# Kernel optimization log

Measured on AMD Instinct MI355X. Metric: run time of the kernel, lower is better.

## Reference

```python
import jax, jax.numpy as jnp
import numpy as np

B = 65536
NREQ = 2097152
NVEH = 1048576
NPAS = 2097152
E = 4194304


def _xavier(key, fi, fo):
    gain = 5.0 / 3.0  # tanh gain
    std = gain * np.sqrt(2.0 / (fi + fo))
    return jax.random.normal(key, (fi, fo), dtype=jnp.float32) * std


def scatter_mean(x, idx, num_segments):
    s = jax.ops.segment_sum(x, idx, num_segments=num_segments)
    c = jax.ops.segment_sum(jnp.ones((x.shape[0], 1), x.dtype), idx, num_segments=num_segments)
    return s / jnp.maximum(c, 1.0)


def setup_inputs() -> dict:
    key = jax.random.key(0)
    ks = jax.random.split(key, 16)
    inp = {
        "requests_x": jax.random.normal(ks[0], (NREQ, 10), dtype=jnp.float32),
        "requests_x_batch": jnp.sort(jax.random.randint(ks[1], (NREQ,), 0, B)),
        "vehicles_x": jax.random.normal(ks[2], (NVEH, 8), dtype=jnp.float32),
        "vehicles_x_batch": jnp.sort(jax.random.randint(ks[3], (NVEH,), 0, B)),
        "passengers_x": jax.random.normal(ks[4], (NPAS, 10), dtype=jnp.float32),
        "veh2pas_receiver_edge_index": jax.random.randint(ks[5], (E,), 0, NPAS),
        "veh2pas_sender_edge_index": jax.random.randint(ks[6], (E,), 0, NVEH),
        "req2veh_receiver_start_index": jax.random.randint(ks[7], (B,), 0, NVEH),
        "W_req": _xavier(ks[8], 10, 16), "b_req": jnp.zeros((16,), jnp.float32),
        "W_veh": _xavier(ks[9], 8, 16), "b_veh": jnp.zeros((16,), jnp.float32),
        "W_pas": _xavier(ks[10], 10, 16), "b_pas": jnp.zeros((16,), jnp.float32),
        "W1": _xavier(ks[11], 64, 64), "b1": jnp.zeros((64,), jnp.float32),
        "W2": _xavier(ks[12], 64, 64), "b2": jnp.zeros((64,), jnp.float32),
        "W3": _xavier(ks[13], 64, 1), "b3": jnp.zeros((1,), jnp.float32),
    }
    return inp


def reference(requests_x, requests_x_batch, vehicles_x, vehicles_x_batch, passengers_x,
              veh2pas_receiver_edge_index, veh2pas_sender_edge_index,
              req2veh_receiver_start_index,
              W_req, b_req, W_veh, b_veh, W_pas, b_pas, W1, b1, W2, b2, W3, b3):
    # per-node-type small MLPs
    req_feat = jnp.tanh(requests_x @ W_req + b_req)            # [NREQ,16]
    req_mean = scatter_mean(req_feat, requests_x_batch, B)      # [B,16]
    veh_feat = jnp.tanh(vehicles_x @ W_veh + b_veh)             # [NVEH,16]
    pas_feat = jnp.tanh(passengers_x @ W_pas + b_pas)           # [NPAS,16]
    # gather passengers along edges, mean-pool onto vehicles
    pas_mean = scatter_mean(pas_feat[veh2pas_receiver_edge_index],
                            veh2pas_sender_edge_index, NVEH)    # [NVEH,16]
    ego_feat = jnp.concatenate([veh_feat, pas_mean], axis=-1)[req2veh_receiver_start_index]  # [B,32]
    veh_mean = scatter_mean(veh_feat, vehicles_x_batch, B)      # [B,16]
    action_feat = jnp.concatenate([req_mean, ego_feat, veh_mean], axis=-1)  # [B,64]
    h = jnp.tanh(action_feat @ W1 + b1)
    h = jnp.tanh(h @ W2 + b2)
    return h @ W3 + b3                                          # [B,1]
```

## Files before the change

### kernel.cpp

```cpp
#include <hip/hip_runtime.h>
#include <cstddef>
#include <cstdint>

#define TPB 256
#define BATCH 65536
#define NREQ 2097152
#define NVEH 1048576
#define NPAS 2097152
#define NEDGE 4194304
#define CAP 32
#define RANK_NEG ((int)0x80808080)

__device__ __forceinline__ float fast_tanh(float x) {
    float e = __expf(2.0f * x);
    return 1.0f - 2.0f / (e + 1.0f);
}
__device__ __forceinline__ float4 tanh4(float4 v) {
    return make_float4(fast_tanh(v.x), fast_tanh(v.y), fast_tanh(v.z), fast_tanh(v.w));
}

__global__ __launch_bounds__(TPB) void k_bounds(
    const int* __restrict__ req_batch, const int* __restrict__ veh_batch,
    const int* __restrict__ req2veh,
    int* __restrict__ seg_req, int* __restrict__ seg_veh,
    unsigned char* __restrict__ mark, int* __restrict__ rank, int* __restrict__ cnt)
{
    int i = blockIdx.x * TPB + threadIdx.x;
    {
        int cur = req_batch[i];
        int prev = (i == 0) ? -1 : req_batch[i - 1];
        for (int b = prev + 1; b <= cur; ++b) seg_req[b] = i;
        if (i == NREQ - 1)
            for (int b = cur + 1; b <= BATCH; ++b) seg_req[b] = NREQ;
    }
    if (i < NVEH) {
        int cur = veh_batch[i];
        int prev = (i == 0) ? -1 : veh_batch[i - 1];
        for (int b = prev + 1; b <= cur; ++b) seg_veh[b] = i;
        if (i == NVEH - 1)
            for (int b = cur + 1; b <= BATCH; ++b) seg_veh[b] = NVEH;
    }
    if (i < BATCH) {
        int v = req2veh[i];
        mark[v] = 1;
        int old = atomicCAS(&rank[v], RANK_NEG, RANK_NEG + 1);
        if (old == RANK_NEG) rank[v] = atomicAdd(cnt, 1);
    }
}

template<int F>
__device__ __forceinline__ void seg_mean_reg(
    const float* __restrict__ x, const int* __restrict__ seg,
    const float* __restrict__ W, const float* __restrict__ bias,
    float* __restrict__ mean_out, int b, int q)
{
    float4 wq[F];
    #pragma unroll
    for (int i = 0; i < F; ++i)
        wq[i] = *reinterpret_cast<const float4*>(&W[i*16 + q*4]);
    float4 bq = reinterpret_cast<const float4*>(bias)[q];

    int lo = seg[b];
    int hi = seg[b + 1];
    float4 s = make_float4(0.f, 0.f, 0.f, 0.f);
    for (int r = lo; r < hi; ++r) {
        float xr[F];
        if constexpr (F == 10) {
            const float2* p2 = reinterpret_cast<const float2*>(x + (size_t)r * 10);
            #pragma unroll
            for (int i = 0; i < 5; ++i) { float2 t = p2[i]; xr[2*i] = t.x; xr[2*i+1] = t.y; }
        } else {
            const float4* p4 = reinterpret_cast<const float4*>(x + (size_t)r * 8);
            float4 t0 = p4[0], t1 = p4[1];
            xr[0]=t0.x; xr[1]=t0.y; xr[2]=t0.z; xr[3]=t0.w;
            xr[4]=t1.x; xr[5]=t1.y; xr[6]=t1.z; xr[7]=t1.w;
        }
        float4 acc = bq;
        #pragma unroll
        for (int i = 0; i < F; ++i) {
            acc.x = fmaf(xr[i], wq[i].x, acc.x);
            acc.y = fmaf(xr[i], wq[i].y, acc.y);
            acc.z = fmaf(xr[i], wq[i].z, acc.z);
            acc.w = fmaf(xr[i], wq[i].w, acc.w);
        }
        float4 t = tanh4(acc);
        s.x += t.x; s.y += t.y; s.z += t.z; s.w += t.w;
    }
    float inv = 1.0f / fmaxf((float)(hi - lo), 1.0f);
    float4 o = make_float4(s.x*inv, s.y*inv, s.z*inv, s.w*inv);
    reinterpret_cast<float4*>(mean_out)[(size_t)b*4 + q] = o;
}

__global__ __launch_bounds__(TPB, 4) void k_phase1(
    const float* __restrict__ requests_x, const int* __restrict__ seg_req,
    const float* __restrict__ vehicles_x, const int* __restrict__ seg_veh,
    const float* __restrict__ W_req, const float* __restrict__ b_req,
    const float* __restrict__ W_veh, const float* __restrict__ b_veh,
    float* __restrict__ req_mean, float* __restrict__ veh_mean)
{
    const int NB_REQ = BATCH * 4 / TPB;
    int blk = blockIdx.x;
    if (blk < NB_REQ) {
        int t = blk * TPB + threadIdx.x;
        seg_mean_reg<10>(requests_x, seg_req, W_req, b_req, req_mean, t >> 2, t & 3);
    } else {
        int t = (blk - NB_REQ) * TPB + threadIdx.x;
        seg_mean_reg<8>(vehicles_x, seg_veh, W_veh, b_veh, veh_mean, t >> 2, t & 3);
    }
}

__global__ __launch_bounds__(TPB) void k_edge(
    const int* __restrict__ send, const int* __restrict__ recv,
    const unsigned char* __restrict__ mark, const int* __restrict__ rank,
    int* __restrict__ deg, int* __restrict__ bucket)
{
    int e = blockIdx.x * TPB + threadIdx.x;
    int v = send[e];
    if (mark[v]) {
        int r = rank[v];
        int slot = atomicAdd(&deg[r], 1);
        if (slot < CAP) bucket[(size_t)r * CAP + slot] = recv[e];
    }
}

__global__ __launch_bounds__(TPB, 3) void k_final(
    const float* __restrict__ req_mean, const float* __restrict__ veh_mean,
    const int* __restrict__ rank, const int* __restrict__ deg,
    const int* __restrict__ bucket, const float* __restrict__ pas_x,
    const float* __restrict__ vehicles_x, const int* __restrict__ req2veh,
    const float* __restrict__ W_veh, const float* __restrict__ b_veh,
    const float* __restrict__ W_pas, const float* __restrict__ b_pas,
    const float* __restrict__ W1, const float* __restrict__ b1,
    const float* __restrict__ W2, const float* __restrict__ b2,
    const float* __restrict__ W3, const float* __restrict__ b3,
    float* __restrict__ out)
{
    __shared__ __align__(16) float sW1[4096];
    __shared__ __align__(16) float sW2[4096];
    __shared__ float sW3[64];
    __shared__ float sb1[64];
    __shared__ float sb2[64];

    int tid = threadIdx.x;
    {
        const float4* s1 = reinterpret_cast<const float4*>(W1);
        const float4* s2 = reinterpret_cast<const float4*>(W2);
        float4* d1 = reinterpret_cast<float4*>(sW1);
        float4* d2 = reinterpret_cast<float4*>(sW2);
        for (int i = tid; i < 1024; i += TPB) { d1[i] = s1[i]; d2[i] = s2[i]; }
        if (tid < 64) { sW3[tid] = W3[tid]; sb1[tid] = b1[tid]; sb2[tid] = b2[tid]; }
    }
    __syncthreads();

    int q = tid & 3;
    int b = blockIdx.x * (TPB / 4) + (tid >> 2);
    int lane = tid & 63;
    int lbase = lane & ~3;

    float a[64];
    {
        const float4* rs = reinterpret_cast<const float4*>(req_mean) + (size_t)b*4;
        const float4* vs = reinterpret_cast<const float4*>(veh_mean) + (size_t)b*4;
        #pragma unroll
        for (int j4 = 0; j4 < 4; ++j4) {
            float4 t = rs[j4];
            a[4*j4+0]=t.x; a[4*j4+1]=t.y; a[4*j4+2]=t.z; a[4*j4+3]=t.w;
            float4 u = vs[j4];
            a[48+4*j4+0]=u.x; a[48+4*j4+1]=u.y; a[48+4*j4+2]=u.z; a[48+4*j4+3]=u.w;
        }
    }
    int v = req2veh[b];

    float4 fv;
    {
        float4 wv[8];
        #pragma unroll
        for (int i = 0; i < 8; ++i)
            wv[i] = *reinterpret_cast<const float4*>(&W_veh[i*16 + q*4]);
        float4 bv = reinterpret_cast<const float4*>(b_veh)[q];
        const float4* vp = reinterpret_cast<const float4*>(vehicles_x + (size_t)v*8);
        float4 t0 = vp[0], t1 = vp[1];
        float vx[8] = {t0.x,t0.y,t0.z,t0.w,t1.x,t1.y,t1.z,t1.w};
        float4 acc = bv;
        #pragma unroll
        for (int i = 0; i < 8; ++i) {
            acc.x = fmaf(vx[i], wv[i].x, acc.x); acc.y = fmaf(vx[i], wv[i].y, acc.y);
            acc.z = fmaf(vx[i], wv[i].z, acc.z); acc.w = fmaf(vx[i], wv[i].w, acc.w);
        }
        fv = tanh4(acc);
    }

    float4 fp;
    {
        float4 wp[10];
        #pragma unroll
        for (int i = 0; i < 10; ++i)
            wp[i] = *reinterpret_cast<const float4*>(&W_pas[i*16 + q*4]);
        float4 bp = reinterpret_cast<const float4*>(b_pas)[q];
        int r = rank[v];
        int d = deg[r];
        int n = min(d, CAP);
        const int* bk = bucket + (size_t)r * CAP;
        float4 ps = make_float4(0.f, 0.f, 0.f, 0.f);
        for (int s = 0; s < n; ++s) {
            int p = bk[s];
            float px[10];
            const float2* pp = reinterpret_cast<const float2*>(pas_x + (size_t)p * 10);
            #pragma unroll
            for (int i = 0; i < 5; ++i) { float2 t = pp[i]; px[2*i] = t.x; px[2*i+1] = t.y; }
            float4 acc = bp;
            #pragma unroll
            for (int i = 0; i < 10; ++i) {
                acc.x = fmaf(px[i], wp[i].x, acc.x); acc.y = fmaf(px[i], wp[i].y, acc.y);
                acc.z = fmaf(px[i], wp[i].z, acc.z); acc.w = fmaf(px[i], wp[i].w, acc.w);
            }
            float4 t = tanh4(acc);
            ps.x += t.x; ps.y += t.y; ps.z += t.z; ps.w += t.w;
        }
        float inv = 1.0f / fmaxf((float)d, 1.0f);
        fp = make_float4(ps.x*inv, ps.y*inv, ps.z*inv, ps.w*inv);
    }

    #pragma unroll
    for (int src = 0; src < 4; ++src) {
        a[16+4*src+0] = __shfl(fv.x, lbase+src);
        a[16+4*src+1] = __shfl(fv.y, lbase+src);
        a[16+4*src+2] = __shfl(fv.z, lbase+src);
        a[16+4*src+3] = __shfl(fv.w, lbase+src);
        a[32+4*src+0] = __shfl(fp.x, lbase+src);
        a[32+4*src+1] = __shfl(fp.y, lbase+src);
        a[32+4*src+2] = __shfl(fp.z, lbase+src);
        a[32+4*src+3] = __shfl(fp.w, lbase+src);
    }

    const float4* W1v = reinterpret_cast<const float4*>(sW1);
    const float4* W2v = reinterpret_cast<const float4*>(sW2);

    float hq[16];
    {
        float4 acc[4];
        #pragma unroll
        for (int jj = 0; jj < 4; ++jj)
            acc[jj] = *reinterpret_cast<const float4*>(&sb1[q*16 + jj*4]);
        #pragma unroll
        for (int k = 0; k < 64; ++k) {
            float ak = a[k];
            #pragma unroll
            for (int jj = 0; jj < 4; ++jj) {
                float4 w = W1v[k*16 + q*4 + jj];
                acc[jj].x = fmaf(ak, w.x, acc[jj].x); acc[jj].y = fmaf(ak, w.y, acc[jj].y);
                acc[jj].z = fmaf(ak, w.z, acc[jj].z); acc[jj].w = fmaf(ak, w.w, acc[jj].w);
            }
        }
        #pragma unroll
        for (int jj = 0; jj < 4; ++jj) {
            float4 t = tanh4(acc[jj]);
            hq[4*jj+0]=t.x; hq[4*jj+1]=t.y; hq[4*jj+2]=t.z; hq[4*jj+3]=t.w;
        }
    }
    #pragma unroll
    for (int src = 0; src < 4; ++src)
        #pragma unroll
        for (int jj = 0; jj < 16; ++jj)
            a[src*16 + jj] = __shfl(hq[jj], lbase + src);

    float o;
    {
        float4 acc[4];
        #pragma unroll
        for (int jj = 0; jj < 4; ++jj)
            acc[jj] = *reinterpret_cast<const float4*>(&sb2[q*16 + jj*4]);
        #pragma unroll
        for (int k = 0; k < 64; ++k) {
            float ak = a[k];
            #pragma unroll
            for (int jj = 0; jj < 4; ++jj) {
                float4 w = W2v[k*16 + q*4 + jj];
                acc[jj].x = fmaf(ak, w.x, acc[jj].x); acc[jj].y = fmaf(ak, w.y, acc[jj].y);
                acc[jj].z = fmaf(ak, w.z, acc[jj].z); acc[jj].w = fmaf(ak, w.w, acc[jj].w);
            }
        }
        o = 0.0f;
        #pragma unroll
        for (int jj = 0; jj < 4; ++jj) {
            float4 t = tanh4(acc[jj]);
            o = fmaf(t.x, sW3[q*16+4*jj+0], o);
            o = fmaf(t.y, sW3[q*16+4*jj+1], o);
            o = fmaf(t.z, sW3[q*16+4*jj+2], o);
            o = fmaf(t.w, sW3[q*16+4*jj+3], o);
        }
    }
    o += __shfl_xor(o, 1);
    o += __shfl_xor(o, 2);
    if (q == 0) out[b] = o + b3[0];
}

extern "C" void kernel_launch(void* const* d_in, const int* in_sizes, int n_in,
                              void* d_out, int out_size, void* d_ws, size_t ws_size,
                              hipStream_t stream) {
    const float* requests_x = (const float*)d_in[0];
    const int*   req_batch  = (const int*)d_in[1];
    const float* vehicles_x = (const float*)d_in[2];
    const int*   veh_batch  = (const int*)d_in[3];
    const float* pas_x      = (const float*)d_in[4];
    const int*   recv       = (const int*)d_in[5];
    const int*   send       = (const int*)d_in[6];
    const int*   req2veh    = (const int*)d_in[7];
    const float* W_req = (const float*)d_in[8];
    const float* b_req = (const float*)d_in[9];
    const float* W_veh = (const float*)d_in[10];
    const float* b_veh = (const float*)d_in[11];
    const float* W_pas = (const float*)d_in[12];
    const float* b_pas = (const float*)d_in[13];
    const float* W1 = (const float*)d_in[14];
    const float* b1 = (const float*)d_in[15];
    const float* W2 = (const float*)d_in[16];
    const float* b2 = (const float*)d_in[17];
    const float* W3 = (const float*)d_in[18];
    const float* b3 = (const float*)d_in[19];
    float* out = (float*)d_out;

    char* ws = (char*)d_ws;
    float*         req_mean = (float*)        (ws + 0);
    float*         veh_mean = (float*)        (ws + (4u<<20));
    int*           seg_req  = (int*)          (ws + (8u<<20));
    int*           seg_veh  = (int*)          (ws + (9u<<20));
    unsigned char* mark     = (unsigned char*)(ws + (10u<<20));
    int*           rank     = (int*)          (ws + (11u<<20));
    int*           deg      = (int*)          (ws + (15u<<20));
    int*           cnt      = (int*)          (ws + (15u<<20) + (256u<<10));
    int*           bucket   = (int*)          (ws + (16u<<20));

    hipMemsetAsync(mark, 0, NVEH, stream);
    hipMemsetAsync(rank, 0x80, NVEH * sizeof(int), stream);
    hipMemsetAsync(deg, 0, (256u<<10) + 64, stream);

    k_bounds<<<NREQ/TPB, TPB, 0, stream>>>(
        req_batch, veh_batch, req2veh, seg_req, seg_veh, mark, rank, cnt);

    k_phase1<<<(BATCH*4/TPB)*2, TPB, 0, stream>>>(
        requests_x, seg_req, vehicles_x, seg_veh,
        W_req, b_req, W_veh, b_veh, req_mean, veh_mean);

    k_edge<<<NEDGE/TPB, TPB, 0, stream>>>(send, recv, mark, rank, deg, bucket);

    k_final<<<BATCH*4/TPB, TPB, 0, stream>>>(
        req_mean, veh_mean, rank, deg, bucket, pas_x,
        vehicles_x, req2veh, W_veh, b_veh, W_pas, b_pas,
        W1, b1, W2, b2, W3, b3, out);
}
```

Measured before the change: 174.4 us.

## Stage segment rows in shared memory and use bitmask for vehicle marks

Phase 1 now has each block cover 64 contiguous segments. It loads their rows cooperatively and coalesced into LDS tiles of 512 rows, and each 4-thread team then reduces its own segment from shared memory. Before, each thread walked its segment's rows with strided global loads. Separately, the per-vehicle byte mark array becomes a packed bitmask set with atomicOr, which shrinks the memset and the random lookups in the edge kernel to 128KB. The costs are extra __syncthreads per tile, atomics when setting bits, and reduced occupancy from LDS use.

```diff
diff --git a/kernel.cpp b/kernel.cpp
--- a/kernel.cpp
+++ b/kernel.cpp
@@ -6,10 +6,11 @@
 #define BATCH 65536
 #define NREQ 2097152
 #define NVEH 1048576
-#define NPAS 2097152
 #define NEDGE 4194304
 #define CAP 32
 #define RANK_NEG ((int)0x80808080)
+#define RT 512
+#define SPB 64
 
 __device__ __forceinline__ float fast_tanh(float x) {
     float e = __expf(2.0f * x);
@@ -23,7 +24,7 @@
     const int* __restrict__ req_batch, const int* __restrict__ veh_batch,
     const int* __restrict__ req2veh,
     int* __restrict__ seg_req, int* __restrict__ seg_veh,
-    unsigned char* __restrict__ mark, int* __restrict__ rank, int* __restrict__ cnt)
+    unsigned* __restrict__ markbits, int* __restrict__ rank, int* __restrict__ cnt)
 {
     int i = blockIdx.x * TPB + threadIdx.x;
     {
@@ -42,81 +43,99 @@
     }
     if (i < BATCH) {
         int v = req2veh[i];
-        mark[v] = 1;
+        atomicOr(&markbits[v >> 5], 1u << (v & 31));
         int old = atomicCAS(&rank[v], RANK_NEG, RANK_NEG + 1);
         if (old == RANK_NEG) rank[v] = atomicAdd(cnt, 1);
     }
 }
 
 template<int F>
-__device__ __forceinline__ void seg_mean_reg(
+__device__ __forceinline__ void phase1_work(
     const float* __restrict__ x, const int* __restrict__ seg,
     const float* __restrict__ W, const float* __restrict__ bias,
-    float* __restrict__ mean_out, int b, int q)
-{
+    float* __restrict__ mout, int b0, float2* sX, int tid)
+{
+    constexpr int FP2 = F / 2;
+    int team = tid >> 2, q = tid & 3;
+    int b = b0 + team;
+    int lo = seg[b], hi = seg[b + 1];
+    int lo0 = seg[b0], hi_all = seg[b0 + SPB];
+
     float4 wq[F];
     #pragma unroll
     for (int i = 0; i < F; ++i)
-        wq[i] = *reinterpret_cast<const float4*>(&W[i*16 + q*4]);
+        wq[i] = *reinterpret_cast<const float4*>(&W[i * 16 + q * 4]);
     float4 bq = reinterpret_cast<const float4*>(bias)[q];
 
-    int lo = seg[b];
-    int hi = seg[b + 1];
     float4 s = make_float4(0.f, 0.f, 0.f, 0.f);
-    for (int r = lo; r < hi; ++r) {
-        float xr[F];
+
+    for (int rb = lo0; rb < hi_all; rb += RT) {
+        int nr = min(RT, hi_all - rb);
+        __syncthreads();
         if constexpr (F == 10) {
-            const float2* p2 = reinterpret_cast<const float2*>(x + (size_t)r * 10);
-            #pragma unroll
-            for (int i = 0; i < 5; ++i) { float2 t = p2[i]; xr[2*i] = t.x; xr[2*i+1] = t.y; }
+            const float2* src = reinterpret_cast<const float2*>(x + (size_t)rb * 10);
+            for (int i = tid; i < nr * 5; i += TPB) sX[i] = src[i];
         } else {
-            const float4* p4 = reinterpret_cast<const float4*>(x + (size_t)r * 8);
-            float4 t0 = p4[0], t1 = p4[1];
-            xr[0]=t0.x; xr[1]=t0.y; xr[2]=t0.z; xr[3]=t0.w;
-            xr[4]=t1.x; xr[5]=t1.y; xr[6]=t1.z; xr[7]=t1.w;
-        }
-        float4 acc = bq;
-        #pragma unroll
-        for (int i = 0; i < F; ++i) {
-            acc.x = fmaf(xr[i], wq[i].x, acc.x);
-            acc.y = fmaf(xr[i], wq[i].y, acc.y);
-            acc.z = fmaf(xr[i], wq[i].z, acc.z);
-            acc.w = fmaf(xr[i], wq[i].w, acc.w);
-        }
-        float4 t = tanh4(acc);
-        s.x += t.x; s.y += t.y; s.z += t.z; s.w += t.w;
+            const float2* src = reinterpret_cast<const float2*>(x + (size_t)rb * 8);
+            for (int idx = tid; idx < nr * 4; idx += TPB) {
+                int rr = idx >> 2, i = idx & 3;
+                sX[rr * 5 + i] = src[idx];
+            }
+        }
+        __syncthreads();
+
+        int r0 = max(lo, rb), r1 = min(hi, rb + nr);
+        for (int r = r0; r < r1; ++r) {
+            const float2* row = &sX[(r - rb) * 5];
+            float xr[F];
+            #pragma unroll
+            for (int i = 0; i < FP2; ++i) {
+                float2 t = row[i];
+                xr[2 * i] = t.x; xr[2 * i + 1] = t.y;
+            }
+            float4 acc = bq;
+            #pragma unroll
+            for (int i = 0; i < F; ++i) {
+                acc.x = fmaf(xr[i], wq[i].x, acc.x);
+                acc.y = fmaf(xr[i], wq[i].y, acc.y);
+                acc.z = fmaf(xr[i], wq[i].z, acc.z);
+                acc.w = fmaf(xr[i], wq[i].w, acc.w);
+            }
+            float4 t = tanh4(acc);
+            s.x += t.x; s.y += t.y; s.z += t.z; s.w += t.w;
+        }
     }
     float inv = 1.0f / fmaxf((float)(hi - lo), 1.0f);
-    float4 o = make_float4(s.x*inv, s.y*inv, s.z*inv, s.w*inv);
-    reinterpret_cast<float4*>(mean_out)[(size_t)b*4 + q] = o;
-}
-
-__global__ __launch_bounds__(TPB, 4) void k_phase1(
+    float4 o = make_float4(s.x * inv, s.y * inv, s.z * inv, s.w * inv);
+    reinterpret_cast<float4*>(mout)[(size_t)b * 4 + q] = o;
+}
+
+__global__ __launch_bounds__(TPB) void k_phase1(
     const float* __restrict__ requests_x, const int* __restrict__ seg_req,
     const float* __restrict__ vehicles_x, const int* __restrict__ seg_veh,
     const float* __restrict__ W_req, const float* __restrict__ b_req,
     const float* __restrict__ W_veh, const float* __restrict__ b_veh,
     float* __restrict__ req_mean, float* __restrict__ veh_mean)
 {
-    const int NB_REQ = BATCH * 4 / TPB;
+    __shared__ __align__(16) float2 sX[RT * 5];
+    const int NBR = BATCH / SPB;
     int blk = blockIdx.x;
-    if (blk < NB_REQ) {
-        int t = blk * TPB + threadIdx.x;
-        seg_mean_reg<10>(requests_x, seg_req, W_req, b_req, req_mean, t >> 2, t & 3);
-    } else {
-        int t = (blk - NB_REQ) * TPB + threadIdx.x;
-        seg_mean_reg<8>(vehicles_x, seg_veh, W_veh, b_veh, veh_mean, t >> 2, t & 3);
-    }
+    if (blk < NBR)
+        phase1_work<10>(requests_x, seg_req, W_req, b_req, req_mean,
+                        blk * SPB, sX, threadIdx.x);
+    else
+        phase1_work<8>(vehicles_x, seg_veh, W_veh, b_veh, veh_mean,
+                       (blk - NBR) * SPB, sX, threadIdx.x);
 }
 
 __global__ __launch_bounds__(TPB) void k_edge(
     const int* __restrict__ send, const int* __restrict__ recv,
-    const unsigned char* __restrict__ mark, const int* __restrict__ rank,
+    const unsigned* __restrict__ markbits, const int* __restrict__ rank,
     int* __restrict__ deg, int* __restrict__ bucket)
 {
     int e = blockIdx.x * TPB + threadIdx.x;
     int v = send[e];
-    if (mark[v]) {
+    if ((markbits[v >> 5] >> (v & 31)) & 1u) {
         int r = rank[v];
         int slot = atomicAdd(&deg[r], 1);
         if (slot < CAP) bucket[(size_t)r * CAP + slot] = recv[e];
@@ -321,28 +340,28 @@
     float* out = (float*)d_out;
 
     char* ws = (char*)d_ws;
-    float*         req_mean = (float*)        (ws + 0);
-    float*         veh_mean = (float*)        (ws + (4u<<20));
-    int*           seg_req  = (int*)          (ws + (8u<<20));
-    int*           seg_veh  = (int*)          (ws + (9u<<20));
-    unsigned char* mark     = (unsigned char*)(ws + (10u<<20));
-    int*           rank     = (int*)          (ws + (11u<<20));
-    int*           deg      = (int*)          (ws + (15u<<20));
-    int*           cnt      = (int*)          (ws + (15u<<20) + (256u<<10));
-    int*           bucket   = (int*)          (ws + (16u<<20));
-
-    hipMemsetAsync(mark, 0, NVEH, stream);
+    float*    req_mean = (float*)   (ws + 0);
+    float*    veh_mean = (float*)   (ws + (4u<<20));
+    int*      seg_req  = (int*)     (ws + (8u<<20));
+    int*      seg_veh  = (int*)     (ws + (9u<<20));
+    unsigned* markbits = (unsigned*)(ws + (10u<<20));
+    int*      rank     = (int*)     (ws + (11u<<20));
+    int*      deg      = (int*)     (ws + (15u<<20));
+    int*      cnt      = (int*)     (ws + (15u<<20) + (256u<<10));
+    int*      bucket   = (int*)     (ws + (16u<<20));
+
+    hipMemsetAsync(markbits, 0, NVEH / 8, stream);
     hipMemsetAsync(rank, 0x80, NVEH * sizeof(int), stream);
     hipMemsetAsync(deg, 0, (256u<<10) + 64, stream);
 
     k_bounds<<<NREQ/TPB, TPB, 0, stream>>>(
-        req_batch, veh_batch, req2veh, seg_req, seg_veh, mark, rank, cnt);
-
-    k_phase1<<<(BATCH*4/TPB)*2, TPB, 0, stream>>>(
+        req_batch, veh_batch, req2veh, seg_req, seg_veh, markbits, rank, cnt);
+
+    k_phase1<<<(BATCH/SPB)*2, TPB, 0, stream>>>(
         requests_x, seg_req, vehicles_x, seg_veh,
         W_req, b_req, W_veh, b_veh, req_mean, veh_mean);
 
-    k_edge<<<NEDGE/TPB, TPB, 0, stream>>>(send, recv, mark, rank, deg, bucket);
+    k_edge<<<NEDGE/TPB, TPB, 0, stream>>>(send, recv, markbits, rank, deg, bucket);
 
     k_final<<<BATCH*4/TPB, TPB, 0, stream>>>(
         req_mean, veh_mean, rank, deg, bucket, pas_x,
```

New measurement: 223.3 us. +28.0%, slower.

## Merge segment-mean and edge kernels, bitmask marks, vectorize loads and unroll gathers

Applied to the files above, without the earlier changes.

Folds the request/vehicle segment-mean kernel and the edge-bucketing kernel into one launch so the two independent phases can run concurrently. The byte mark array becomes a bitmask set with atomicOr, which shrinks the memset and the lookup footprint. The bounds and edge kernels now process four items per thread with int4 loads. The segment-mean and passenger-gather loops are unrolled by four to get more loads in flight. The cost is more register pressure, extra atomics on shared bitmask words, and a new workspace layout.

```diff
diff --git a/kernel.cpp b/kernel.cpp
--- a/kernel.cpp
+++ b/kernel.cpp
@@ -6,7 +6,6 @@
 #define BATCH 65536
 #define NREQ 2097152
 #define NVEH 1048576
-#define NPAS 2097152
 #define NEDGE 4194304
 #define CAP 32
 #define RANK_NEG ((int)0x80808080)
@@ -17,34 +16,64 @@
 }
 __device__ __forceinline__ float4 tanh4(float4 v) {
     return make_float4(fast_tanh(v.x), fast_tanh(v.y), fast_tanh(v.z), fast_tanh(v.w));
+}
+
+template<int F>
+__device__ __forceinline__ void load_row(const float* __restrict__ x, int r, float* xr) {
+    if constexpr (F == 10) {
+        const float2* p = reinterpret_cast<const float2*>(x + (size_t)r * 10);
+        #pragma unroll
+        for (int i = 0; i < 5; ++i) { float2 t = p[i]; xr[2*i] = t.x; xr[2*i+1] = t.y; }
+    } else {
+        const float4* p = reinterpret_cast<const float4*>(x + (size_t)r * 8);
+        float4 a = p[0], b = p[1];
+        xr[0]=a.x; xr[1]=a.y; xr[2]=a.z; xr[3]=a.w;
+        xr[4]=b.x; xr[5]=b.y; xr[6]=b.z; xr[7]=b.w;
+    }
 }
 
 __global__ __launch_bounds__(TPB) void k_bounds(
     const int* __restrict__ req_batch, const int* __restrict__ veh_batch,
     const int* __restrict__ req2veh,
     int* __restrict__ seg_req, int* __restrict__ seg_veh,
-    unsigned char* __restrict__ mark, int* __restrict__ rank, int* __restrict__ cnt)
+    unsigned* __restrict__ markbits, int* __restrict__ rank, int* __restrict__ cnt)
 {
-    int i = blockIdx.x * TPB + threadIdx.x;
-    {
-        int cur = req_batch[i];
-        int prev = (i == 0) ? -1 : req_batch[i - 1];
-        for (int b = prev + 1; b <= cur; ++b) seg_req[b] = i;
-        if (i == NREQ - 1)
-            for (int b = cur + 1; b <= BATCH; ++b) seg_req[b] = NREQ;
-    }
-    if (i < NVEH) {
-        int cur = veh_batch[i];
-        int prev = (i == 0) ? -1 : veh_batch[i - 1];
-        for (int b = prev + 1; b <= cur; ++b) seg_veh[b] = i;
-        if (i == NVEH - 1)
-            for (int b = cur + 1; b <= BATCH; ++b) seg_veh[b] = NVEH;
-    }
-    if (i < BATCH) {
-        int v = req2veh[i];
-        mark[v] = 1;
-        int old = atomicCAS(&rank[v], RANK_NEG, RANK_NEG + 1);
-        if (old == RANK_NEG) rank[v] = atomicAdd(cnt, 1);
+    int t = blockIdx.x * TPB + threadIdx.x;
+    int i0 = t * 4;
+    {
+        int4 c = *reinterpret_cast<const int4*>(req_batch + i0);
+        int prev = (i0 == 0) ? -1 : req_batch[i0 - 1];
+        int vals[4] = {c.x, c.y, c.z, c.w};
+        #pragma unroll
+        for (int u = 0; u < 4; ++u) {
+            for (int b = prev + 1; b <= vals[u]; ++b) seg_req[b] = i0 + u;
+            prev = vals[u];
+        }
+        if (i0 + 4 == NREQ)
+            for (int b = prev + 1; b <= BATCH; ++b) seg_req[b] = NREQ;
+    }
+    if (i0 < NVEH) {
+        int4 c = *reinterpret_cast<const int4*>(veh_batch + i0);
+        int prev = (i0 == 0) ? -1 : veh_batch[i0 - 1];
+        int vals[4] = {c.x, c.y, c.z, c.w};
+        #pragma unroll
+        for (int u = 0; u < 4; ++u) {
+            for (int b = prev + 1; b <= vals[u]; ++b) seg_veh[b] = i0 + u;
+            prev = vals[u];
+        }
+        if (i0 + 4 == NVEH)
+            for (int b = prev + 1; b <= BATCH; ++b) seg_veh[b] = NVEH;
+    }
+    if (i0 < BATCH) {
+        int4 vv = *reinterpret_cast<const int4*>(req2veh + i0);
+        int vs[4] = {vv.x, vv.y, vv.z, vv.w};
+        #pragma unroll
+        for (int u = 0; u < 4; ++u) {
+            int v = vs[u];
+            atomicOr(&markbits[v >> 5], 1u << (v & 31));
+            int old = atomicCAS(&rank[v], RANK_NEG, RANK_NEG + 1);
+            if (old == RANK_NEG) rank[v] = atomicAdd(cnt, 1);
+        }
     }
 }
 
@@ -63,18 +92,29 @@
     int lo = seg[b];
     int hi = seg[b + 1];
     float4 s = make_float4(0.f, 0.f, 0.f, 0.f);
-    for (int r = lo; r < hi; ++r) {
+
+    int r = lo;
+    for (; r + 4 <= hi; r += 4) {
+        float xr[4][F];
+        #pragma unroll
+        for (int u = 0; u < 4; ++u) load_row<F>(x, r + u, xr[u]);
+        #pragma unroll
+        for (int u = 0; u < 4; ++u) {
+            float4 acc = bq;
+            #pragma unroll
+            for (int i = 0; i < F; ++i) {
+                acc.x = fmaf(xr[u][i], wq[i].x, acc.x);
+                acc.y = fmaf(xr[u][i], wq[i].y, acc.y);
+                acc.z = fmaf(xr[u][i], wq[i].z, acc.z);
+                acc.w = fmaf(xr[u][i], wq[i].w, acc.w);
+            }
+            float4 tv = tanh4(acc);
+            s.x += tv.x; s.y += tv.y; s.z += tv.z; s.w += tv.w;
+        }
+    }
+    for (; r < hi; ++r) {
         float xr[F];
-        if constexpr (F == 10) {
-            const float2* p2 = reinterpret_cast<const float2*>(x + (size_t)r * 10);
-            #pragma unroll
-            for (int i = 0; i < 5; ++i) { float2 t = p2[i]; xr[2*i] = t.x; xr[2*i+1] = t.y; }
-        } else {
-            const float4* p4 = reinterpret_cast<const float4*>(x + (size_t)r * 8);
-            float4 t0 = p4[0], t1 = p4[1];
-            xr[0]=t0.x; xr[1]=t0.y; xr[2]=t0.z; xr[3]=t0.w;
-            xr[4]=t1.x; xr[5]=t1.y; xr[6]=t1.z; xr[7]=t1.w;
-        }
+        load_row<F>(x, r, xr);
         float4 acc = bq;
         #pragma unroll
         for (int i = 0; i < F; ++i) {
@@ -83,43 +123,50 @@
             acc.z = fmaf(xr[i], wq[i].z, acc.z);
             acc.w = fmaf(xr[i], wq[i].w, acc.w);
         }
-        float4 t = tanh4(acc);
-        s.x += t.x; s.y += t.y; s.z += t.z; s.w += t.w;
+        float4 tv = tanh4(acc);
+        s.x += tv.x; s.y += tv.y; s.z += tv.z; s.w += tv.w;
     }
     float inv = 1.0f / fmaxf((float)(hi - lo), 1.0f);
     float4 o = make_float4(s.x*inv, s.y*inv, s.z*inv, s.w*inv);
     reinterpret_cast<float4*>(mean_out)[(size_t)b*4 + q] = o;
 }
 
-__global__ __launch_bounds__(TPB, 4) void k_phase1(
+#define NB_REQ (BATCH/64)
+#define NB_VEH (BATCH/64)
+#define NB_P1  (NB_REQ + NB_VEH)
+#define NB_EDGE (NEDGE/(TPB*4))
+
+__global__ __launch_bounds__(TPB, 4) void k_mid(
     const float* __restrict__ requests_x, const int* __restrict__ seg_req,
     const float* __restrict__ vehicles_x, const int* __restrict__ seg_veh,
     const float* __restrict__ W_req, const float* __restrict__ b_req,
     const float* __restrict__ W_veh, const float* __restrict__ b_veh,
-    float* __restrict__ req_mean, float* __restrict__ veh_mean)
-{
-    const int NB_REQ = BATCH * 4 / TPB;
-    int blk = blockIdx.x;
-    if (blk < NB_REQ) {
-        int t = blk * TPB + threadIdx.x;
-        seg_mean_reg<10>(requests_x, seg_req, W_req, b_req, req_mean, t >> 2, t & 3);
-    } else {
-        int t = (blk - NB_REQ) * TPB + threadIdx.x;
-        seg_mean_reg<8>(vehicles_x, seg_veh, W_veh, b_veh, veh_mean, t >> 2, t & 3);
-    }
-}
-
-__global__ __launch_bounds__(TPB) void k_edge(
+    float* __restrict__ req_mean, float* __restrict__ veh_mean,
     const int* __restrict__ send, const int* __restrict__ recv,
-    const unsigned char* __restrict__ mark, const int* __restrict__ rank,
+    const unsigned* __restrict__ markbits, const int* __restrict__ rank,
     int* __restrict__ deg, int* __restrict__ bucket)
 {
-    int e = blockIdx.x * TPB + threadIdx.x;
-    int v = send[e];
-    if (mark[v]) {
-        int r = rank[v];
-        int slot = atomicAdd(&deg[r], 1);
-        if (slot < CAP) bucket[(size_t)r * CAP + slot] = recv[e];
+    int blk = blockIdx.x;
+    int tid = threadIdx.x;
+    if (blk < NB_REQ) {
+        int t = blk * TPB + tid;
+        seg_mean_reg<10>(requests_x, seg_req, W_req, b_req, req_mean, t >> 2, t & 3);
+    } else if (blk < NB_P1) {
+        int t = (blk - NB_REQ) * TPB + tid;
+        seg_mean_reg<8>(vehicles_x, seg_veh, W_veh, b_veh, veh_mean, t >> 2, t & 3);
+    } else {
+        int e4 = (blk - NB_P1) * TPB + tid;
+        int4 sv = reinterpret_cast<const int4*>(send)[e4];
+        int vv[4] = {sv.x, sv.y, sv.z, sv.w};
+        #pragma unroll
+        for (int u = 0; u < 4; ++u) {
+            int v = vv[u];
+            if ((markbits[v >> 5] >> (v & 31)) & 1u) {
+                int rk = rank[v];
+                int slot = atomicAdd(&deg[rk], 1);
+                if (slot < CAP) bucket[(size_t)rk * CAP + slot] = recv[e4 * 4 + u];
+            }
+        }
     }
 }
 
@@ -178,9 +225,8 @@
         for (int i = 0; i < 8; ++i)
             wv[i] = *reinterpret_cast<const float4*>(&W_veh[i*16 + q*4]);
         float4 bv = reinterpret_cast<const float4*>(b_veh)[q];
-        const float4* vp = reinterpret_cast<const float4*>(vehicles_x + (size_t)v*8);
-        float4 t0 = vp[0], t1 = vp[1];
-        float vx[8] = {t0.x,t0.y,t0.z,t0.w,t1.x,t1.y,t1.z,t1.w};
+        float vx[8];
+        load_row<8>(vehicles_x, v, vx);
         float4 acc = bv;
         #pragma unroll
         for (int i = 0; i < 8; ++i) {
@@ -200,22 +246,31 @@
         int r = rank[v];
         int d = deg[r];
         int n = min(d, CAP);
-        const int* bk = bucket + (size_t)r * CAP;
+        const int4* bk4 = reinterpret_cast<const int4*>(bucket + (size_t)r * CAP);
         float4 ps = make_float4(0.f, 0.f, 0.f, 0.f);
-        for (int s = 0; s < n; ++s) {
-            int p = bk[s];
-            float px[10];
-            const float2* pp = reinterpret_cast<const float2*>(pas_x + (size_t)p * 10);
+        for (int c = 0; c * 4 < n; ++c) {
+            int4 idx = bk4[c];
+            int pv[4] = {idx.x, idx.y, idx.z, idx.w};
+            int m = n - c * 4;
+            float px[4][10];
             #pragma unroll
-            for (int i = 0; i < 5; ++i) { float2 t = pp[i]; px[2*i] = t.x; px[2*i+1] = t.y; }
-            float4 acc = bp;
+            for (int u = 0; u < 4; ++u)
+                if (u < m) load_row<10>(pas_x, pv[u], px[u]);
             #pragma unroll
-            for (int i = 0; i < 10; ++i) {
-                acc.x = fmaf(px[i], wp[i].x, acc.x); acc.y = fmaf(px[i], wp[i].y, acc.y);
-                acc.z = fmaf(px[i], wp[i].z, acc.z); acc.w = fmaf(px[i], wp[i].w, acc.w);
+            for (int u = 0; u < 4; ++u) {
+                if (u < m) {
+                    float4 acc = bp;
+                    #pragma unroll
+                    for (int i = 0; i < 10; ++i) {
+                        acc.x = fmaf(px[u][i], wp[i].x, acc.x);
+                        acc.y = fmaf(px[u][i], wp[i].y, acc.y);
+                        acc.z = fmaf(px[u][i], wp[i].z, acc.z);
+                        acc.w = fmaf(px[u][i], wp[i].w, acc.w);
+                    }
+                    float4 t = tanh4(acc);
+                    ps.x += t.x; ps.y += t.y; ps.z += t.z; ps.w += t.w;
+                }
             }
-            float4 t = tanh4(acc);
-            ps.x += t.x; ps.y += t.y; ps.z += t.z; ps.w += t.w;
         }
         float inv = 1.0f / fmaxf((float)d, 1.0f);
         fp = make_float4(ps.x*inv, ps.y*inv, ps.z*inv, ps.w*inv);
@@ -321,28 +376,26 @@
     float* out = (float*)d_out;
 
     char* ws = (char*)d_ws;
-    float*         req_mean = (float*)        (ws + 0);
-    float*         veh_mean = (float*)        (ws + (4u<<20));
-    int*           seg_req  = (int*)          (ws + (8u<<20));
-    int*           seg_veh  = (int*)          (ws + (9u<<20));
-    unsigned char* mark     = (unsigned char*)(ws + (10u<<20));
-    int*           rank     = (int*)          (ws + (11u<<20));
-    int*           deg      = (int*)          (ws + (15u<<20));
-    int*           cnt      = (int*)          (ws + (15u<<20) + (256u<<10));
-    int*           bucket   = (int*)          (ws + (16u<<20));
-
-    hipMemsetAsync(mark, 0, NVEH, stream);
+    float*    req_mean = (float*)   (ws + 0);
+    float*    veh_mean = (float*)   (ws + (4u<<20));
+    int*      seg_req  = (int*)     (ws + (8u<<20));
+    int*      seg_veh  = (int*)     (ws + (9u<<20));
+    unsigned* markbits = (unsigned*)(ws + (10u<<20));
+    int*      deg      = (int*)     (ws + (10u<<20) + (128u<<10));
+    int*      cnt      = (int*)     (ws + (10u<<20) + (384u<<10));
+    int*      rank     = (int*)     (ws + (11u<<20));
+    int*      bucket   = (int*)     (ws + (15u<<20));
+
+    hipMemsetAsync(markbits, 0, (384u<<10) + 64, stream);
     hipMemsetAsync(rank, 0x80, NVEH * sizeof(int), stream);
-    hipMemsetAsync(deg, 0, (256u<<10) + 64, stream);
-
-    k_bounds<<<NREQ/TPB, TPB, 0, stream>>>(
-        req_batch, veh_batch, req2veh, seg_req, seg_veh, mark, rank, cnt);
-
-    k_phase1<<<(BATCH*4/TPB)*2, TPB, 0, stream>>>(
+
+    k_bounds<<<NREQ/4/TPB, TPB, 0, stream>>>(
+        req_batch, veh_batch, req2veh, seg_req, seg_veh, markbits, rank, cnt);
+
+    k_mid<<<NB_P1 + NB_EDGE, TPB, 0, stream>>>(
         requests_x, seg_req, vehicles_x, seg_veh,
-        W_req, b_req, W_veh, b_veh, req_mean, veh_mean);
-
-    k_edge<<<NEDGE/TPB, TPB, 0, stream>>>(send, recv, mark, rank, deg, bucket);
+        W_req, b_req, W_veh, b_veh, req_mean, veh_mean,
+        send, recv, markbits, rank, deg, bucket);
 
     k_final<<<BATCH*4/TPB, TPB, 0, stream>>>(
         req_mean, veh_mean, rank, deg, bucket, pas_x,
```

Result: faster. 165.8 us (-4.9%).
